# Optimization experiments

Hardware: AMD Instinct MI355X
Metric: run time of the kernel (lower is better)

The kernel has to match this reference:

```python
import jax, jax.numpy as jnp
import numpy as np
from jax.scipy.linalg import expm

D = 512      # d_model
S = 3        # num_scales
BATCH = 256
H = 8        # attention heads
HD = D // H  # head dim


def layernorm(x, g, b, eps=1e-5):
    m = jnp.mean(x, axis=-1, keepdims=True)
    v = jnp.var(x, axis=-1, keepdims=True)
    return (x - m) / jnp.sqrt(v + eps) * g + b


def setup_inputs() -> dict:
    key = jax.random.key(0)
    ks = jax.random.split(key, 16)
    sd = 1.0 / np.sqrt(D)
    inp = {
        'x': jax.random.normal(ks[0], (BATCH, D), jnp.float32),
        'h_prev': jax.random.normal(ks[1], (BATCH, D), jnp.float32),
        'lstm_h': jax.random.normal(ks[2], (S, BATCH, D), jnp.float32) * 0.1,
        'lstm_c': jax.random.normal(ks[3], (S, BATCH, D), jnp.float32) * 0.1,
        'A': jax.random.normal(ks[4], (D, D), jnp.float32) * sd,
        'Bm': jax.random.normal(ks[5], (D, D), jnp.float32) * sd,
        'dn_w1': jax.random.normal(ks[6], (D, D), jnp.float32) * sd,
        'dn_b1': jnp.zeros((D,), jnp.float32),
        'dn_g': jnp.ones((D,), jnp.float32),
        'dn_beta': jnp.zeros((D,), jnp.float32),
        'dn_w2': jax.random.normal(ks[7], (1, D), jnp.float32) * sd,
        'dn_b2': jnp.zeros((1,), jnp.float32),
        'lstm_wih': jax.random.normal(ks[8], (S, 4 * D, D), jnp.float32) * sd,
        'lstm_whh': jax.random.normal(ks[9], (S, 4 * D, D), jnp.float32) * sd,
        'lstm_bih': jnp.zeros((S, 4 * D), jnp.float32),
        'lstm_bhh': jnp.zeros((S, 4 * D), jnp.float32),
        'decays': jnp.linspace(0.5, 0.95, S, dtype=jnp.float32),
        'attn_in_w': jax.random.normal(ks[10], (3 * D, D), jnp.float32) * sd,
        'attn_in_b': jnp.zeros((3 * D,), jnp.float32),
        'attn_out_w': jax.random.normal(ks[11], (D, D), jnp.float32) * sd,
        'attn_out_b': jnp.zeros((D,), jnp.float32),
        'proj_w': jax.random.normal(ks[12], (D, (S + 2) * D), jnp.float32) * (1.0 / np.sqrt((S + 2) * D)),
        'proj_b': jnp.zeros((D,), jnp.float32),
        'proj_g': jnp.ones((D,), jnp.float32),
        'proj_beta': jnp.zeros((D,), jnp.float32),
    }
    return inp


def reference(x, h_prev, lstm_h, lstm_c, A, Bm, dn_w1, dn_b1, dn_g, dn_beta,
              dn_w2, dn_b2, lstm_wih, lstm_whh, lstm_bih, lstm_bhh, decays,
              attn_in_w, attn_in_b, attn_out_w, attn_out_b,
              proj_w, proj_b, proj_g, proj_beta):
    # ---- delta_net: Linear -> LayerNorm -> GELU(exact) -> Linear -> Softplus ----
    h1 = layernorm(x @ dn_w1.T + dn_b1, dn_g, dn_beta)
    h1 = jax.nn.gelu(h1, approximate=False)
    delta = jax.nn.softplus(h1 @ dn_w2.T + dn_b2)           # (B, 1)

    # ---- SSM update: h_t = expm(delta*A) h_prev + delta*B x ----
    A_disc = jax.vmap(expm)(delta[:, :, None] * A)          # (B, D, D)
    h_ssm = jnp.einsum('bij,bj->bi', A_disc, h_prev) + delta * jnp.einsum('ij,bj->bi', Bm, x)

    # ---- multi-scale LSTM cells (vectorized over scales) ----
    gates = (jnp.einsum('bd,skd->sbk', x, lstm_wih)
             + jnp.einsum('sbd,skd->sbk', lstm_h, lstm_whh)
             + (lstm_bih + lstm_bhh)[:, None, :])           # (S, B, 4D)
    gi, gf, gg, go = jnp.split(gates, 4, axis=-1)
    i_g = jax.nn.sigmoid(gi)
    f_g = jax.nn.sigmoid(gf)
    g_g = jnp.tanh(gg)
    o_g = jax.nn.sigmoid(go)
    c_raw = f_g * lstm_c + i_g * g_g                        # (S, B, D)
    h_new = o_g * jnp.tanh(c_raw)                           # (S, B, D)
    dec = decays[:, None, None]
    c_new = dec * lstm_c + (1.0 - dec) * c_raw              # (S, B, D)

    # ---- fusion attention: 1 query (h_ssm), S keys/values (h_new) ----
    Wq, Wk, Wv = jnp.split(attn_in_w, 3, axis=0)
    bq, bk, bv = jnp.split(attn_in_b, 3, axis=0)
    kv = jnp.transpose(h_new, (1, 0, 2))                    # (B, S, D)
    q = (h_ssm @ Wq.T + bq).reshape(-1, 1, H, HD).transpose(0, 2, 1, 3)   # (B,H,1,HD)
    k = (kv @ Wk.T + bk).reshape(-1, S, H, HD).transpose(0, 2, 1, 3)      # (B,H,S,HD)
    v = (kv @ Wv.T + bv).reshape(-1, S, H, HD).transpose(0, 2, 1, 3)
    scores = jnp.einsum('bhqe,bhke->bhqk', q, k) / np.sqrt(HD)
    attn = jax.nn.softmax(scores, axis=-1)
    ctx = jnp.einsum('bhqk,bhke->bhqe', attn, v)            # (B,H,1,HD)
    ctx = ctx.transpose(0, 2, 1, 3).reshape(-1, D)          # (B, D)
    fused = ctx @ attn_out_w.T + attn_out_b                 # (B, D)

    # ---- output projection over concat [h_ssm, fused, h_1..h_S] ----
    combined = jnp.concatenate([h_ssm, fused] + [h_new[i] for i in range(S)], axis=-1)
    output = layernorm(combined @ proj_w.T + proj_b, proj_g, proj_beta)
    return (output, h_ssm, h_new, c_new)
```

## Files before the change

### kernel.cpp

```cpp
#include <hip/hip_runtime.h>
#include <math.h>

#define DIM 512
#define NS 3
#define NB 256
#define KMAX 24

using bf16x8 = __attribute__((ext_vector_type(8))) short;
using f32x4  = __attribute__((ext_vector_type(4))) float;
using float4v = __attribute__((ext_vector_type(4))) float;

__device__ __forceinline__ unsigned short f2b(float f) {
    union { float f; unsigned int u; } v; v.f = f;
    unsigned int r = v.u + 0x7fffu + ((v.u >> 16) & 1u);
    return (unsigned short)(r >> 16);
}
__device__ __forceinline__ float b2f(unsigned short u) {
    union { unsigned int u; float f; } v; v.u = ((unsigned int)u) << 16;
    return v.f;
}

struct GemmDesc {
    const unsigned short* X;
    const unsigned short* W;
    const float* bias;
    float* Cf;
    unsigned short* Cb;
    unsigned short* Ct;
    int M, N, K, ldX, ldC, tr_row0;
};
struct GemmArgs { GemmDesc d[4]; };

__global__ __launch_bounds__(256) void gemm_mfma(GemmArgs args)
{
    GemmDesc de = args.d[blockIdx.y];
    int tn = de.N >> 6;
    int tiles = (de.M >> 6) * tn;
    int t = blockIdx.x;
    if (t >= tiles) return;
    int m0 = (t / tn) << 6;
    int n0 = (t % tn) << 6;

    __shared__ unsigned short lsA[2][4096];
    __shared__ unsigned short lsB[2][4096];

    int tid = threadIdx.x;
    int w = tid >> 6;
    int l = tid & 63;

    int nkt = de.K >> 6;

    int srow = w * 16 + (l >> 2);
    int schk = l & 3;
    const unsigned short* gA = de.X + (size_t)(m0 + srow) * de.ldX + schk * 8;
    const unsigned short* gB = de.W + (size_t)(n0 + srow) * de.K  + schk * 8;
    unsigned short* lA = &lsA[0][(w * 64 + l) * 8];
    unsigned short* lB = &lsB[0][(w * 64 + l) * 8];

#define STAGE(bufi, kt)                                                          \
    do {                                                                         \
        __builtin_amdgcn_global_load_lds(                                        \
            (const __attribute__((address_space(1))) unsigned int*)(gA + (size_t)(kt) * 64), \
            (__attribute__((address_space(3))) unsigned int*)(lA + (bufi) * 4096), 16, 0, 0); \
        __builtin_amdgcn_global_load_lds(                                        \
            (const __attribute__((address_space(1))) unsigned int*)(gA + (size_t)(kt) * 64 + 32), \
            (__attribute__((address_space(3))) unsigned int*)(lA + (bufi) * 4096 + 2048), 16, 0, 0); \
        __builtin_amdgcn_global_load_lds(                                        \
            (const __attribute__((address_space(1))) unsigned int*)(gB + (size_t)(kt) * 64), \
            (__attribute__((address_space(3))) unsigned int*)(lB + (bufi) * 4096), 16, 0, 0); \
        __builtin_amdgcn_global_load_lds(                                        \
            (const __attribute__((address_space(1))) unsigned int*)(gB + (size_t)(kt) * 64 + 32), \
            (__attribute__((address_space(3))) unsigned int*)(lB + (bufi) * 4096 + 2048), 16, 0, 0); \
    } while (0)

    int mbase = (w >> 1) * 32;
    int nbase = (w & 1) * 32;

    f32x4 acc[2][2];
    #pragma unroll
    for (int i = 0; i < 2; ++i)
        #pragma unroll
        for (int j = 0; j < 2; ++j)
            acc[i][j] = (f32x4){0.f, 0.f, 0.f, 0.f};

    int kg = l >> 4;
    int fr = l & 15;
    int aslot = (mbase * 4 + fr * 4 + kg) * 8;
    int bslot = (nbase * 4 + fr * 4 + kg) * 8;

    STAGE(0, 0);

    for (int kt = 0; kt < nkt; ++kt) {
        __syncthreads();
        if (kt + 1 < nkt) STAGE((kt + 1) & 1, kt + 1);

        const unsigned short* bufA = &lsA[kt & 1][0];
        const unsigned short* bufB = &lsB[kt & 1][0];
        #pragma unroll
        for (int h = 0; h < 2; ++h) {
            bf16x8 a0 = *(const bf16x8*)(bufA + h * 2048 + aslot);
            bf16x8 a1 = *(const bf16x8*)(bufA + h * 2048 + aslot + 512);
            bf16x8 b0 = *(const bf16x8*)(bufB + h * 2048 + bslot);
            bf16x8 b1 = *(const bf16x8*)(bufB + h * 2048 + bslot + 512);
            acc[0][0] = __builtin_amdgcn_mfma_f32_16x16x32_bf16(a0, b0, acc[0][0], 0, 0, 0);
            acc[0][1] = __builtin_amdgcn_mfma_f32_16x16x32_bf16(a0, b1, acc[0][1], 0, 0, 0);
            acc[1][0] = __builtin_amdgcn_mfma_f32_16x16x32_bf16(a1, b0, acc[1][0], 0, 0, 0);
            acc[1][1] = __builtin_amdgcn_mfma_f32_16x16x32_bf16(a1, b1, acc[1][1], 0, 0, 0);
        }
    }

    #pragma unroll
    for (int mi = 0; mi < 2; ++mi) {
        #pragma unroll
        for (int ni = 0; ni < 2; ++ni) {
            int col = n0 + nbase + ni * 16 + fr;
            float bv = de.bias ? de.bias[col] : 0.f;
            #pragma unroll
            for (int r = 0; r < 4; ++r) {
                int row = m0 + mbase + mi * 16 + (l >> 4) * 4 + r;
                float v = acc[mi][ni][r] + bv;
                if (de.Cf) de.Cf[(size_t)row * de.ldC + col] = v;
                else       de.Cb[(size_t)row * de.ldC + col] = f2b(v);
                if (de.Ct && row >= de.tr_row0)
                    de.Ct[(size_t)col * 512 + (row - de.tr_row0)] = f2b(v);
            }
        }
    }
#undef STAGE
}

struct ConvArgs { const float* s[8]; unsigned short* d[8]; int n4[8]; int nseg; };
__global__ void convert_pairs(ConvArgs a)
{
    int stride = gridDim.x * blockDim.x;
    for (int seg = 0; seg < a.nseg; ++seg) {
        const float4v* src = (const float4v*)a.s[seg];
        unsigned short* dst = a.d[seg];
        int n4 = a.n4[seg];
        for (int i = blockIdx.x * blockDim.x + threadIdx.x; i < n4; i += stride) {
            float4v v = src[i];
            dst[i*4+0] = f2b(v.x); dst[i*4+1] = f2b(v.y);
            dst[i*4+2] = f2b(v.z); dst[i*4+3] = f2b(v.w);
        }
    }
}

__global__ void build_lstm_cat(const float* __restrict__ wih, const float* __restrict__ whh,
                               const float* __restrict__ x, const float* __restrict__ lh,
                               unsigned short* __restrict__ Wcat, unsigned short* __restrict__ Xcat)
{
    int stride = gridDim.x * blockDim.x;
    const int W4 = 3 * 2048 * 256;
    const int X4 = 3 * 256 * 256;
    for (int g = blockIdx.x * blockDim.x + threadIdx.x; g < W4; g += stride) {
        int s = g / 524288;
        int rr = g - s * 524288;
        int r = rr >> 8;
        int c = (rr & 255) * 4;
        const float* src = (c < 512) ? (wih + (size_t)s * 1048576 + (size_t)r * 512 + c)
                                     : (whh + (size_t)s * 1048576 + (size_t)r * 512 + (c - 512));
        float4v v = *(const float4v*)src;
        unsigned short* dst = Wcat + (size_t)s * 2097152 + (size_t)r * 1024 + c;
        dst[0] = f2b(v.x); dst[1] = f2b(v.y); dst[2] = f2b(v.z); dst[3] = f2b(v.w);
    }
    for (int g = blockIdx.x * blockDim.x + threadIdx.x; g < X4; g += stride) {
        int s = g / 65536;
        int rr = g - s * 65536;
        int b = rr >> 8;
        int c = (rr & 255) * 4;
        const float* src = (c < 512) ? (x + (size_t)b * 512 + c)
                                     : (lh + (size_t)s * 131072 + (size_t)b * 512 + (c - 512));
        float4v v = *(const float4v*)src;
        unsigned short* dst = Xcat + (size_t)s * 262144 + (size_t)b * 1024 + c;
        dst[0] = f2b(v.x); dst[1] = f2b(v.y); dst[2] = f2b(v.z); dst[3] = f2b(v.w);
    }
}

__global__ void transposeA_bf16(const float* __restrict__ A, unsigned short* __restrict__ ATb)
{
    __shared__ float tile[32][33];
    int x = blockIdx.x * 32 + threadIdx.x;
    int y = blockIdx.y * 32 + threadIdx.y;
    #pragma unroll
    for (int i = 0; i < 32; i += 8)
        tile[threadIdx.y + i][threadIdx.x] = A[(size_t)(y + i) * DIM + x];
    __syncthreads();
    x = blockIdx.y * 32 + threadIdx.x;
    y = blockIdx.x * 32 + threadIdx.y;
    #pragma unroll
    for (int i = 0; i < 32; i += 8)
        ATb[(size_t)(y + i) * DIM + x] = f2b(tile[threadIdx.x][threadIdx.y + i]);
}

__device__ __forceinline__ void block_reduce2(float& s, float& q, float* sb1, float* sb2)
{
    int tid = threadIdx.x;
    #pragma unroll
    for (int off = 32; off > 0; off >>= 1) {
        s += __shfl_down(s, off);
        q += __shfl_down(q, off);
    }
    if ((tid & 63) == 0) { sb1[tid >> 6] = s; sb2[tid >> 6] = q; }
    __syncthreads();
    s = sb1[0] + sb1[1] + sb1[2] + sb1[3];
    q = sb2[0] + sb2[1] + sb2[2] + sb2[3];
    __syncthreads();
}

__global__ __launch_bounds__(256) void ln_gelu_delta(
    const float* __restrict__ pre, const float* __restrict__ g,
    const float* __restrict__ beta, const float* __restrict__ w2,
    const float* __restrict__ b2, float* __restrict__ delta,
    float* __restrict__ coeff)
{
    __shared__ float sb1[4], sb2[4];
    int b = blockIdx.x, tid = threadIdx.x;
    int i0 = tid, i1 = tid + 256;
    float x0 = pre[(size_t)b * DIM + i0];
    float x1 = pre[(size_t)b * DIM + i1];
    float s = x0 + x1, q = x0 * x0 + x1 * x1;
    block_reduce2(s, q, sb1, sb2);
    float mean = s * (1.f / DIM);
    float var  = q * (1.f / DIM) - mean * mean;
    float inv  = rsqrtf(var + 1e-5f);
    float y0 = (x0 - mean) * inv * g[i0] + beta[i0];
    float y1 = (x1 - mean) * inv * g[i1] + beta[i1];
    float h0 = 0.5f * y0 * (1.f + erff(y0 * 0.70710678118654752f));
    float h1 = 0.5f * y1 * (1.f + erff(y1 * 0.70710678118654752f));
    float p = h0 * w2[i0] + h1 * w2[i1];
    float dummy = 0.f;
    block_reduce2(p, dummy, sb1, sb2);
    if (tid == 0) {
        float z = p + b2[0];
        float d = (z > 20.f) ? z : log1pf(expf(z));
        delta[b] = d;
        float c = 1.f;
        coeff[b] = 1.f;
        for (int k = 1; k <= KMAX; ++k) { c *= d / (float)k; coeff[k * 256 + b] = c; }
    }
}

__global__ void taylor_accum(
    const float* __restrict__ T, const float* __restrict__ coeff,
    const float* __restrict__ h_prev, const float* __restrict__ delta,
    const float* __restrict__ Bx, float* __restrict__ hssm,
    unsigned short* __restrict__ combb)
{
    int idx = blockIdx.x * 256 + threadIdx.x;
    int b = idx >> 9, i = idx & 511;
    const float* Tr = T + (size_t)b * (KMAX * DIM) + i;
    float a = h_prev[idx];
    #pragma unroll
    for (int k = 1; k <= KMAX; ++k)
        a += coeff[k * 256 + b] * Tr[(size_t)(k - 1) * DIM];
    float h = a + delta[b] * Bx[idx];
    hssm[idx] = h;
    combb[(size_t)b * 2560 + i] = f2b(h);
}

__global__ void lstm_cell(
    const float* __restrict__ gates, const float* __restrict__ bih,
    const float* __restrict__ bhh, const float* __restrict__ cin,
    const float* __restrict__ decays,
    float* __restrict__ hout, float* __restrict__ cout,
    unsigned short* __restrict__ combb)
{
    int idx = blockIdx.x * 256 + threadIdx.x;
    int s = idx / (NB * DIM);
    int r = idx - s * (NB * DIM);
    int b = r >> 9, d = r & 511;
    const float* gr = gates + (size_t)s * 524288 + (size_t)b * 2048;
    const float* bi = bih + s * 2048;
    const float* bh = bhh + s * 2048;
    float gi = gr[d]        + bi[d]        + bh[d];
    float gf = gr[512 + d]  + bi[512 + d]  + bh[512 + d];
    float gg = gr[1024 + d] + bi[1024 + d] + bh[1024 + d];
    float go = gr[1536 + d] + bi[1536 + d] + bh[1536 + d];
    float ig = 1.f / (1.f + expf(-gi));
    float fg = 1.f / (1.f + expf(-gf));
    float g_ = tanhf(gg);
    float og = 1.f / (1.f + expf(-go));
    float c  = cin[idx];
    float craw = fg * c + ig * g_;
    float hn = og * tanhf(craw);
    float dec = decays[s];
    hout[idx] = hn;
    cout[idx] = dec * c + (1.f - dec) * craw;
    combb[(size_t)b * 2560 + 1024 + s * 512 + d] = f2b(hn);
}

__global__ __launch_bounds__(64) void attn_kernel(
    const unsigned short* __restrict__ qb, const unsigned short* __restrict__ kvb,
    unsigned short* __restrict__ ctxb)
{
    int bh = blockIdx.x;
    int b = bh >> 3, h = bh & 7;
    int e = threadIdx.x;
    int col = h * 64 + e;
    float qe = b2f(qb[(size_t)b * 512 + col]);
    float p0 = qe * b2f(kvb[0 * 262144 + (size_t)b * 1024 + col]);
    float p1 = qe * b2f(kvb[1 * 262144 + (size_t)b * 1024 + col]);
    float p2 = qe * b2f(kvb[2 * 262144 + (size_t)b * 1024 + col]);
    #pragma unroll
    for (int off = 32; off > 0; off >>= 1) {
        p0 += __shfl_xor(p0, off);
        p1 += __shfl_xor(p1, off);
        p2 += __shfl_xor(p2, off);
    }
    const float scale = 0.125f;
    p0 *= scale; p1 *= scale; p2 *= scale;
    float m = fmaxf(p0, fmaxf(p1, p2));
    float w0 = expf(p0 - m), w1 = expf(p1 - m), w2 = expf(p2 - m);
    float invs = 1.f / (w0 + w1 + w2);
    float v0 = b2f(kvb[0 * 262144 + (size_t)b * 1024 + 512 + col]);
    float v1 = b2f(kvb[1 * 262144 + (size_t)b * 1024 + 512 + col]);
    float v2 = b2f(kvb[2 * 262144 + (size_t)b * 1024 + 512 + col]);
    ctxb[(size_t)b * 512 + col] = f2b((w0 * v0 + w1 * v1 + w2 * v2) * invs);
}

__global__ __launch_bounds__(256) void layernorm_k(
    const float* __restrict__ in, const float* __restrict__ g,
    const float* __restrict__ beta, float* __restrict__ outp)
{
    __shared__ float sb1[4], sb2[4];
    int b = blockIdx.x, tid = threadIdx.x;
    int i0 = tid, i1 = tid + 256;
    float x0 = in[(size_t)b * DIM + i0];
    float x1 = in[(size_t)b * DIM + i1];
    float s = x0 + x1, q = x0 * x0 + x1 * x1;
    block_reduce2(s, q, sb1, sb2);
    float mean = s * (1.f / DIM);
    float var  = q * (1.f / DIM) - mean * mean;
    float inv  = rsqrtf(var + 1e-5f);
    outp[(size_t)b * DIM + i0] = (x0 - mean) * inv * g[i0] + beta[i0];
    outp[(size_t)b * DIM + i1] = (x1 - mean) * inv * g[i1] + beta[i1];
}

extern "C" void kernel_launch(void* const* d_in, const int* in_sizes, int n_in,
                              void* d_out, int out_size, void* d_ws, size_t ws_size,
                              hipStream_t stream)
{
    const float* x        = (const float*)d_in[0];
    const float* h_prev   = (const float*)d_in[1];
    const float* lstm_h   = (const float*)d_in[2];
    const float* lstm_c   = (const float*)d_in[3];
    const float* A        = (const float*)d_in[4];
    const float* Bm       = (const float*)d_in[5];
    const float* dn_w1    = (const float*)d_in[6];
    const float* dn_b1    = (const float*)d_in[7];
    const float* dn_g     = (const float*)d_in[8];
    const float* dn_beta  = (const float*)d_in[9];
    const float* dn_w2    = (const float*)d_in[10];
    const float* dn_b2    = (const float*)d_in[11];
    const float* wih      = (const float*)d_in[12];
    const float* whh      = (const float*)d_in[13];
    const float* bih      = (const float*)d_in[14];
    const float* bhh      = (const float*)d_in[15];
    const float* decays   = (const float*)d_in[16];
    const float* ain_w    = (const float*)d_in[17];
    const float* ain_b    = (const float*)d_in[18];
    const float* aout_w   = (const float*)d_in[19];
    const float* aout_b   = (const float*)d_in[20];
    const float* proj_w   = (const float*)d_in[21];
    const float* proj_b   = (const float*)d_in[22];
    const float* proj_g   = (const float*)d_in[23];
    const float* proj_bt  = (const float*)d_in[24];

    float* out  = (float*)d_out;
    float* hssm = out + 131072;
    float* hnew = out + 262144;
    float* cnew = out + 655360;

    unsigned short* us = (unsigned short*)d_ws;
    unsigned short* xb      = us;
    unsigned short* hpb     = us + 131072;
    unsigned short* ATb     = us + 262144;
    unsigned short* dn_w1b  = us + 524288;
    unsigned short* Bmb     = us + 786432;
    unsigned short* ain_wb  = us + 1048576;
    unsigned short* aout_wb = us + 1835008;
    unsigned short* proj_wb = us + 2097152;
    unsigned short* Pw      = us + 3407872;
    unsigned short* Qa      = us + 9699328;
    unsigned short* Qb      = us + 9961472;
    unsigned short* Wcat    = us + 10223616;
    unsigned short* Xcat    = us + 16515072;
    unsigned short* combb   = us + 17301504;
    unsigned short* kvb     = us + 17956864;
    unsigned short* qb      = us + 18743296;
    unsigned short* ctxb    = us + 18874368;
    float* fbase = (float*)(us + 19005440);
    float* pre1   = fbase;
    float* delta  = fbase + 131072;
    float* coeff  = fbase + 131328;
    float* Bx     = fbase + 137728;
    float* Tm     = fbase + 268800;
    float* gates  = Tm;
    float* projout = pre1;

    ConvArgs ca;
    ca.s[0] = x;      ca.d[0] = xb;      ca.n4[0] = 131072/4;
    ca.s[1] = h_prev; ca.d[1] = hpb;     ca.n4[1] = 131072/4;
    ca.s[2] = A;      ca.d[2] = Pw;      ca.n4[2] = 262144/4;
    ca.s[3] = dn_w1;  ca.d[3] = dn_w1b;  ca.n4[3] = 262144/4;
    ca.s[4] = Bm;     ca.d[4] = Bmb;     ca.n4[4] = 262144/4;
    ca.s[5] = ain_w;  ca.d[5] = ain_wb;  ca.n4[5] = 786432/4;
    ca.s[6] = aout_w; ca.d[6] = aout_wb; ca.n4[6] = 262144/4;
    ca.s[7] = proj_w; ca.d[7] = proj_wb; ca.n4[7] = 1310720/4;
    ca.nseg = 8;
    convert_pairs<<<1024, 256, 0, stream>>>(ca);
    build_lstm_cat<<<2048, 256, 0, stream>>>(wih, whh, x, lstm_h, Wcat, Xcat);
    transposeA_bf16<<<dim3(16, 16), dim3(32, 8), 0, stream>>>(A, ATb);

    GemmArgs ga;
    ga.d[0] = { xb, dn_w1b, dn_b1, pre1, nullptr, nullptr, 256, 512, 512, 512, 512, 0 };
    ga.d[1] = { xb, Bmb,    nullptr, Bx,  nullptr, nullptr, 256, 512, 512, 512, 512, 0 };
    gemm_mfma<<<dim3(32, 2), 256, 0, stream>>>(ga);
    ln_gelu_delta<<<256, 256, 0, stream>>>(pre1, dn_g, dn_beta, dn_w2, dn_b2, delta, coeff);

    ga.d[0] = { Pw, ATb, nullptr, nullptr, Pw + 1*262144, Qa, 512, 512, 512, 512, 512, 0 };
    gemm_mfma<<<dim3(64, 1), 256, 0, stream>>>(ga);
    ga.d[0] = { Pw, Qa, nullptr, nullptr, Pw + 2*262144, Qb, 1024, 512, 512, 512, 512, 512 };
    gemm_mfma<<<dim3(128, 1), 256, 0, stream>>>(ga);
    ga.d[0] = { Pw, Qb, nullptr, nullptr, Pw + 4*262144, Qa, 2048, 512, 512, 512, 512, 1536 };
    gemm_mfma<<<dim3(256, 1), 256, 0, stream>>>(ga);
    ga.d[0] = { Pw, Qa, nullptr, nullptr, Pw + 8*262144, Qb, 4096, 512, 512, 512, 512, 3584 };
    gemm_mfma<<<dim3(512, 1), 256, 0, stream>>>(ga);
    ga.d[0] = { Pw, Qb, nullptr, nullptr, Pw + 16*262144, nullptr, 4096, 512, 512, 512, 512, 0 };
    gemm_mfma<<<dim3(512, 1), 256, 0, stream>>>(ga);

    ga.d[0] = { hpb, Pw, nullptr, Tm, nullptr, nullptr, 256, KMAX*512, 512, 512, KMAX*512, 0 };
    gemm_mfma<<<dim3(768, 1), 256, 0, stream>>>(ga);
    taylor_accum<<<512, 256, 0, stream>>>(Tm, coeff, h_prev, delta, Bx, hssm, combb);

    for (int s = 0; s < 3; ++s)
        ga.d[s] = { Xcat + (size_t)s * 262144, Wcat + (size_t)s * 2097152, nullptr,
                    gates + (size_t)s * 524288, nullptr, nullptr, 256, 2048, 1024, 1024, 2048, 0 };
    gemm_mfma<<<dim3(128, 3), 256, 0, stream>>>(ga);
    lstm_cell<<<1536, 256, 0, stream>>>(gates, bih, bhh, lstm_c, decays, hnew, cnew, combb);

    ga.d[0] = { combb, ain_wb, ain_b, nullptr, qb, nullptr, 256, 512, 512, 2560, 512, 0 };
    for (int s = 0; s < 3; ++s)
        ga.d[1 + s] = { combb + 1024 + (size_t)s * 512, ain_wb + 262144, ain_b + 512,
                        nullptr, kvb + (size_t)s * 262144, nullptr, 256, 1024, 512, 2560, 1024, 0 };
    gemm_mfma<<<dim3(64, 4), 256, 0, stream>>>(ga);
    attn_kernel<<<2048, 64, 0, stream>>>(qb, kvb, ctxb);
    ga.d[0] = { ctxb, aout_wb, aout_b, nullptr, combb + 512, nullptr, 256, 512, 512, 512, 2560, 0 };
    gemm_mfma<<<dim3(32, 1), 256, 0, stream>>>(ga);

    ga.d[0] = { combb, proj_wb, proj_b, projout, nullptr, nullptr, 256, 512, 2560, 2560, 512, 0 };
    gemm_mfma<<<dim3(32, 1), 256, 0, stream>>>(ga);
    layernorm_k<<<256, 256, 0, stream>>>(projout, proj_g, proj_bt, out);
}
```

Measured before the change: 273.1 us.

## Cut Taylor order, fold attention out-proj into output projection, merge launches

```diff
diff --git a/kernel.cpp b/kernel.cpp
--- a/kernel.cpp
+++ b/kernel.cpp
@@ -2,9 +2,8 @@
 #include <math.h>
 
 #define DIM 512
-#define NS 3
 #define NB 256
-#define KMAX 24
+#define KMAX 16
 
 using bf16x8 = __attribute__((ext_vector_type(8))) short;
 using f32x4  = __attribute__((ext_vector_type(4))) float;
@@ -47,7 +46,6 @@
     int tid = threadIdx.x;
     int w = tid >> 6;
     int l = tid & 63;
-
     int nkt = de.K >> 6;
 
     int srow = w * 16 + (l >> 2);
@@ -129,18 +127,64 @@
 #undef STAGE
 }
 
-struct ConvArgs { const float* s[8]; unsigned short* d[8]; int n4[8]; int nseg; };
-__global__ void convert_pairs(ConvArgs a)
-{
-    int stride = gridDim.x * blockDim.x;
-    for (int seg = 0; seg < a.nseg; ++seg) {
-        const float4v* src = (const float4v*)a.s[seg];
-        unsigned short* dst = a.d[seg];
-        int n4 = a.n4[seg];
-        for (int i = blockIdx.x * blockDim.x + threadIdx.x; i < n4; i += stride) {
-            float4v v = src[i];
-            dst[i*4+0] = f2b(v.x); dst[i*4+1] = f2b(v.y);
-            dst[i*4+2] = f2b(v.z); dst[i*4+3] = f2b(v.w);
+struct PrepArgs {
+    const float* lin_s[7]; unsigned short* lin_d[7];
+    int lin_n4[7]; int lin_dRL[7]; int lin_sRL[7]; int lin_sOff[7];
+    const float* A; unsigned short* ATb;
+    const float* aout_w; unsigned short* aout_wT;
+    const float* proj_w; const float* proj_b; const float* aout_b; float* bprime;
+};
+__global__ __launch_bounds__(256) void prep_kernel(PrepArgs a)
+{
+    __shared__ float tile[32][33];
+    int bid = blockIdx.x, tid = threadIdx.x;
+    if (bid < 1024) {
+        int gstride = 1024 * 256;
+        int g0 = bid * 256 + tid;
+        for (int seg = 0; seg < 7; ++seg) {
+            int n4 = a.lin_n4[seg];
+            const float* s = a.lin_s[seg];
+            unsigned short* d = a.lin_d[seg];
+            int dRL = a.lin_dRL[seg], sRL = a.lin_sRL[seg], off = a.lin_sOff[seg];
+            if (dRL == sRL && off == 0) {
+                for (int i = g0; i < n4; i += gstride) {
+                    float4v v = ((const float4v*)s)[i];
+                    d[i*4+0] = f2b(v.x); d[i*4+1] = f2b(v.y);
+                    d[i*4+2] = f2b(v.z); d[i*4+3] = f2b(v.w);
+                }
+            } else {
+                for (int i = g0; i < n4; i += gstride) {
+                    int r = i / dRL, c = i - r * dRL;
+                    float4v v = *(const float4v*)(s + ((size_t)r * sRL + off + c) * 4);
+                    unsigned short* dd = d + ((size_t)r * dRL + c) * 4;
+                    dd[0] = f2b(v.x); dd[1] = f2b(v.y); dd[2] = f2b(v.z); dd[3] = f2b(v.w);
+                }
+            }
+        }
+    } else if (bid < 1536) {
+        int t = bid - 1024;
+        const float* src = (t < 256) ? a.A : a.aout_w;
+        unsigned short* dst = (t < 256) ? a.ATb : a.aout_wT;
+        int tt = t & 255;
+        int bx = tt & 15, by = tt >> 4;
+        int tx = tid & 31, ty = tid >> 5;
+        #pragma unroll
+        for (int i = 0; i < 32; i += 8)
+            tile[ty + i][tx] = src[(size_t)(by * 32 + ty + i) * 512 + bx * 32 + tx];
+        __syncthreads();
+        #pragma unroll
+        for (int i = 0; i < 32; i += 8)
+            dst[(size_t)(bx * 32 + ty + i) * 512 + by * 32 + tx] = f2b(tile[tx][ty + i]);
+    } else {
+        int gw = (bid - 1536) * 4 + (tid >> 6);
+        int lane = tid & 63;
+        for (int i = gw; i < 512; i += 32) {
+            float acc = 0.f;
+            for (int n = lane; n < 512; n += 64)
+                acc += a.proj_w[(size_t)i * 2560 + 512 + n] * a.aout_b[n];
+            #pragma unroll
+            for (int off = 32; off > 0; off >>= 1) acc += __shfl_down(acc, off);
+            if (lane == 0) a.bprime[i] = a.proj_b[i] + acc;
         }
     }
 }
@@ -174,22 +218,6 @@
         unsigned short* dst = Xcat + (size_t)s * 262144 + (size_t)b * 1024 + c;
         dst[0] = f2b(v.x); dst[1] = f2b(v.y); dst[2] = f2b(v.z); dst[3] = f2b(v.w);
     }
-}
-
-__global__ void transposeA_bf16(const float* __restrict__ A, unsigned short* __restrict__ ATb)
-{
-    __shared__ float tile[32][33];
-    int x = blockIdx.x * 32 + threadIdx.x;
-    int y = blockIdx.y * 32 + threadIdx.y;
-    #pragma unroll
-    for (int i = 0; i < 32; i += 8)
-        tile[threadIdx.y + i][threadIdx.x] = A[(size_t)(y + i) * DIM + x];
-    __syncthreads();
-    x = blockIdx.y * 32 + threadIdx.x;
-    y = blockIdx.x * 32 + threadIdx.y;
-    #pragma unroll
-    for (int i = 0; i < 32; i += 8)
-        ATb[(size_t)(y + i) * DIM + x] = f2b(tile[threadIdx.x][threadIdx.y + i]);
 }
 
 __device__ __forceinline__ void block_reduce2(float& s, float& q, float* sb1, float* sb2)
@@ -240,58 +268,56 @@
     }
 }
 
-__global__ void taylor_accum(
-    const float* __restrict__ T, const float* __restrict__ coeff,
+__global__ void pointwise_fused(
+    const float* __restrict__ Tm, const float* __restrict__ coeff,
     const float* __restrict__ h_prev, const float* __restrict__ delta,
     const float* __restrict__ Bx, float* __restrict__ hssm,
-    unsigned short* __restrict__ combb)
-{
-    int idx = blockIdx.x * 256 + threadIdx.x;
-    int b = idx >> 9, i = idx & 511;
-    const float* Tr = T + (size_t)b * (KMAX * DIM) + i;
-    float a = h_prev[idx];
-    #pragma unroll
-    for (int k = 1; k <= KMAX; ++k)
-        a += coeff[k * 256 + b] * Tr[(size_t)(k - 1) * DIM];
-    float h = a + delta[b] * Bx[idx];
-    hssm[idx] = h;
-    combb[(size_t)b * 2560 + i] = f2b(h);
-}
-
-__global__ void lstm_cell(
+    unsigned short* __restrict__ combb,
     const float* __restrict__ gates, const float* __restrict__ bih,
     const float* __restrict__ bhh, const float* __restrict__ cin,
     const float* __restrict__ decays,
-    float* __restrict__ hout, float* __restrict__ cout,
-    unsigned short* __restrict__ combb)
+    float* __restrict__ hout, float* __restrict__ cout)
 {
     int idx = blockIdx.x * 256 + threadIdx.x;
-    int s = idx / (NB * DIM);
-    int r = idx - s * (NB * DIM);
-    int b = r >> 9, d = r & 511;
-    const float* gr = gates + (size_t)s * 524288 + (size_t)b * 2048;
-    const float* bi = bih + s * 2048;
-    const float* bh = bhh + s * 2048;
-    float gi = gr[d]        + bi[d]        + bh[d];
-    float gf = gr[512 + d]  + bi[512 + d]  + bh[512 + d];
-    float gg = gr[1024 + d] + bi[1024 + d] + bh[1024 + d];
-    float go = gr[1536 + d] + bi[1536 + d] + bh[1536 + d];
-    float ig = 1.f / (1.f + expf(-gi));
-    float fg = 1.f / (1.f + expf(-gf));
-    float g_ = tanhf(gg);
-    float og = 1.f / (1.f + expf(-go));
-    float c  = cin[idx];
-    float craw = fg * c + ig * g_;
-    float hn = og * tanhf(craw);
-    float dec = decays[s];
-    hout[idx] = hn;
-    cout[idx] = dec * c + (1.f - dec) * craw;
-    combb[(size_t)b * 2560 + 1024 + s * 512 + d] = f2b(hn);
+    if (idx < 131072) {
+        int b = idx >> 9, i = idx & 511;
+        const float* Tr = Tm + (size_t)b * (KMAX * DIM) + i;
+        float a = h_prev[idx];
+        #pragma unroll
+        for (int k = 1; k <= KMAX; ++k)
+            a += coeff[k * 256 + b] * Tr[(size_t)(k - 1) * DIM];
+        float h = a + delta[b] * Bx[idx];
+        hssm[idx] = h;
+        combb[(size_t)b * 2560 + i] = f2b(h);
+    } else {
+        int idx2 = idx - 131072;
+        int s = idx2 / (NB * DIM);
+        int r = idx2 - s * (NB * DIM);
+        int b = r >> 9, d = r & 511;
+        const float* gr = gates + (size_t)s * 524288 + (size_t)b * 2048;
+        const float* bi = bih + s * 2048;
+        const float* bh = bhh + s * 2048;
+        float gi = gr[d]        + bi[d]        + bh[d];
+        float gf = gr[512 + d]  + bi[512 + d]  + bh[512 + d];
+        float gg = gr[1024 + d] + bi[1024 + d] + bh[1024 + d];
+        float go = gr[1536 + d] + bi[1536 + d] + bh[1536 + d];
+        float ig = 1.f / (1.f + expf(-gi));
+        float fg = 1.f / (1.f + expf(-gf));
+        float g_ = tanhf(gg);
+        float og = 1.f / (1.f + expf(-go));
+        float c  = cin[idx2];
+        float craw = fg * c + ig * g_;
+        float hn = og * tanhf(craw);
+        float dec = decays[s];
+        hout[idx2] = hn;
+        cout[idx2] = dec * c + (1.f - dec) * craw;
+        combb[(size_t)b * 2560 + 1024 + s * 512 + d] = f2b(hn);
+    }
 }
 
 __global__ __launch_bounds__(64) void attn_kernel(
     const unsigned short* __restrict__ qb, const unsigned short* __restrict__ kvb,
-    unsigned short* __restrict__ ctxb)
+    unsigned short* __restrict__ combb)
 {
     int bh = blockIdx.x;
     int b = bh >> 3, h = bh & 7;
@@ -315,7 +341,7 @@
     float v0 = b2f(kvb[0 * 262144 + (size_t)b * 1024 + 512 + col]);
     float v1 = b2f(kvb[1 * 262144 + (size_t)b * 1024 + 512 + col]);
     float v2 = b2f(kvb[2 * 262144 + (size_t)b * 1024 + 512 + col]);
-    ctxb[(size_t)b * 512 + col] = f2b((w0 * v0 + w1 * v1 + w2 * v2) * invs);
+    combb[(size_t)b * 2560 + 512 + col] = f2b((w0 * v0 + w1 * v1 + w2 * v2) * invs);
 }
 
 __global__ __launch_bounds__(256) void layernorm_k(
@@ -372,50 +398,51 @@
     float* cnew = out + 655360;
 
     unsigned short* us = (unsigned short*)d_ws;
-    unsigned short* xb      = us;
-    unsigned short* hpb     = us + 131072;
-    unsigned short* ATb     = us + 262144;
-    unsigned short* dn_w1b  = us + 524288;
-    unsigned short* Bmb     = us + 786432;
-    unsigned short* ain_wb  = us + 1048576;
-    unsigned short* aout_wb = us + 1835008;
-    unsigned short* proj_wb = us + 2097152;
-    unsigned short* Pw      = us + 3407872;
-    unsigned short* Qa      = us + 9699328;
-    unsigned short* Qb      = us + 9961472;
-    unsigned short* Wcat    = us + 10223616;
-    unsigned short* Xcat    = us + 16515072;
-    unsigned short* combb   = us + 17301504;
-    unsigned short* kvb     = us + 17956864;
-    unsigned short* qb      = us + 18743296;
-    unsigned short* ctxb    = us + 18874368;
-    float* fbase = (float*)(us + 19005440);
+    unsigned short* hpb     = us;
+    unsigned short* ATb     = us + 131072;
+    unsigned short* dn_w1b  = us + 393216;
+    unsigned short* Bmb     = us + 655360;
+    unsigned short* ain_wb  = us + 917504;
+    unsigned short* proj_wb = us + 1703936;
+    unsigned short* P2b     = us + 3014656;
+    unsigned short* aout_wT = us + 3276800;
+    unsigned short* Pw      = us + 3538944;
+    unsigned short* Qa      = us + 7733248;
+    unsigned short* Qb      = us + 7995392;
+    unsigned short* Wcat    = us + 8257536;
+    unsigned short* Xcat    = us + 14548992;
+    unsigned short* combb   = us + 15335424;
+    unsigned short* qb      = us + 15990784;
+    unsigned short* kvb     = us + 16121856;
+    float* fbase  = (float*)(us + 16908288);
     float* pre1   = fbase;
     float* delta  = fbase + 131072;
     float* coeff  = fbase + 131328;
-    float* Bx     = fbase + 137728;
-    float* Tm     = fbase + 268800;
-    float* gates  = Tm;
+    float* Bx     = fbase + 135680;
+    float* bprime = fbase + 266752;
+    float* Tm     = fbase + 267264;
+    float* gates  = fbase + 2364416;
     float* projout = pre1;
 
-    ConvArgs ca;
-    ca.s[0] = x;      ca.d[0] = xb;      ca.n4[0] = 131072/4;
-    ca.s[1] = h_prev; ca.d[1] = hpb;     ca.n4[1] = 131072/4;
-    ca.s[2] = A;      ca.d[2] = Pw;      ca.n4[2] = 262144/4;
-    ca.s[3] = dn_w1;  ca.d[3] = dn_w1b;  ca.n4[3] = 262144/4;
-    ca.s[4] = Bm;     ca.d[4] = Bmb;     ca.n4[4] = 262144/4;
-    ca.s[5] = ain_w;  ca.d[5] = ain_wb;  ca.n4[5] = 786432/4;
-    ca.s[6] = aout_w; ca.d[6] = aout_wb; ca.n4[6] = 262144/4;
-    ca.s[7] = proj_w; ca.d[7] = proj_wb; ca.n4[7] = 1310720/4;
-    ca.nseg = 8;
-    convert_pairs<<<1024, 256, 0, stream>>>(ca);
+    PrepArgs pa;
+    pa.lin_s[0] = h_prev; pa.lin_d[0] = hpb;     pa.lin_n4[0] = 32768;  pa.lin_dRL[0]=1;   pa.lin_sRL[0]=1;   pa.lin_sOff[0]=0;
+    pa.lin_s[1] = A;      pa.lin_d[1] = Pw;      pa.lin_n4[1] = 65536;  pa.lin_dRL[1]=1;   pa.lin_sRL[1]=1;   pa.lin_sOff[1]=0;
+    pa.lin_s[2] = dn_w1;  pa.lin_d[2] = dn_w1b;  pa.lin_n4[2] = 65536;  pa.lin_dRL[2]=1;   pa.lin_sRL[2]=1;   pa.lin_sOff[2]=0;
+    pa.lin_s[3] = Bm;     pa.lin_d[3] = Bmb;     pa.lin_n4[3] = 65536;  pa.lin_dRL[3]=1;   pa.lin_sRL[3]=1;   pa.lin_sOff[3]=0;
+    pa.lin_s[4] = ain_w;  pa.lin_d[4] = ain_wb;  pa.lin_n4[4] = 196608; pa.lin_dRL[4]=1;   pa.lin_sRL[4]=1;   pa.lin_sOff[4]=0;
+    pa.lin_s[5] = proj_w; pa.lin_d[5] = proj_wb; pa.lin_n4[5] = 327680; pa.lin_dRL[5]=1;   pa.lin_sRL[5]=1;   pa.lin_sOff[5]=0;
+    pa.lin_s[6] = proj_w; pa.lin_d[6] = P2b;     pa.lin_n4[6] = 65536;  pa.lin_dRL[6]=128; pa.lin_sRL[6]=640; pa.lin_sOff[6]=128;
+    pa.A = A; pa.ATb = ATb; pa.aout_w = aout_w; pa.aout_wT = aout_wT;
+    pa.proj_w = proj_w; pa.proj_b = proj_b; pa.aout_b = aout_b; pa.bprime = bprime;
+    prep_kernel<<<1544, 256, 0, stream>>>(pa);
     build_lstm_cat<<<2048, 256, 0, stream>>>(wih, whh, x, lstm_h, Wcat, Xcat);
-    transposeA_bf16<<<dim3(16, 16), dim3(32, 8), 0, stream>>>(A, ATb);
 
     GemmArgs ga;
-    ga.d[0] = { xb, dn_w1b, dn_b1, pre1, nullptr, nullptr, 256, 512, 512, 512, 512, 0 };
-    ga.d[1] = { xb, Bmb,    nullptr, Bx,  nullptr, nullptr, 256, 512, 512, 512, 512, 0 };
-    gemm_mfma<<<dim3(32, 2), 256, 0, stream>>>(ga);
+    ga.d[0] = { Xcat, dn_w1b, dn_b1, pre1, nullptr, nullptr, 256, 512, 512, 1024, 512, 0 };
+    ga.d[1] = { Xcat, Bmb,    nullptr, Bx,  nullptr, nullptr, 256, 512, 512, 1024, 512, 0 };
+    ga.d[2] = { P2b,  aout_wT, nullptr, nullptr, proj_wb + 512, nullptr, 512, 512, 512, 512, 2560, 0 };
+    ga.d[3] = ga.d[0];
+    gemm_mfma<<<dim3(64, 3), 256, 0, stream>>>(ga);
     ln_gelu_delta<<<256, 256, 0, stream>>>(pre1, dn_g, dn_beta, dn_w2, dn_b2, delta, coeff);
 
     ga.d[0] = { Pw, ATb, nullptr, nullptr, Pw + 1*262144, Qa, 512, 512, 512, 512, 512, 0 };
@@ -424,31 +451,26 @@
     gemm_mfma<<<dim3(128, 1), 256, 0, stream>>>(ga);
     ga.d[0] = { Pw, Qb, nullptr, nullptr, Pw + 4*262144, Qa, 2048, 512, 512, 512, 512, 1536 };
     gemm_mfma<<<dim3(256, 1), 256, 0, stream>>>(ga);
-    ga.d[0] = { Pw, Qa, nullptr, nullptr, Pw + 8*262144, Qb, 4096, 512, 512, 512, 512, 3584 };
+    ga.d[0] = { Pw, Qa, nullptr, nullptr, Pw + 8*262144, nullptr, 4096, 512, 512, 512, 512, 0 };
     gemm_mfma<<<dim3(512, 1), 256, 0, stream>>>(ga);
-    ga.d[0] = { Pw, Qb, nullptr, nullptr, Pw + 16*262144, nullptr, 4096, 512, 512, 512, 512, 0 };
-    gemm_mfma<<<dim3(512, 1), 256, 0, stream>>>(ga);
 
     ga.d[0] = { hpb, Pw, nullptr, Tm, nullptr, nullptr, 256, KMAX*512, 512, 512, KMAX*512, 0 };
-    gemm_mfma<<<dim3(768, 1), 256, 0, stream>>>(ga);
-    taylor_accum<<<512, 256, 0, stream>>>(Tm, coeff, h_prev, delta, Bx, hssm, combb);
-
     for (int s = 0; s < 3; ++s)
-        ga.d[s] = { Xcat + (size_t)s * 262144, Wcat + (size_t)s * 2097152, nullptr,
-                    gates + (size_t)s * 524288, nullptr, nullptr, 256, 2048, 1024, 1024, 2048, 0 };
-    gemm_mfma<<<dim3(128, 3), 256, 0, stream>>>(ga);
-    lstm_cell<<<1536, 256, 0, stream>>>(gates, bih, bhh, lstm_c, decays, hnew, cnew, combb);
+        ga.d[1 + s] = { Xcat + (size_t)s * 262144, Wcat + (size_t)s * 2097152, nullptr,
+                        gates + (size_t)s * 524288, nullptr, nullptr, 256, 2048, 1024, 1024, 2048, 0 };
+    gemm_mfma<<<dim3(512, 4), 256, 0, stream>>>(ga);
+
+    pointwise_fused<<<2048, 256, 0, stream>>>(Tm, coeff, h_prev, delta, Bx, hssm, combb,
+                                              gates, bih, bhh, lstm_c, decays, hnew, cnew);
 
     ga.d[0] = { combb, ain_wb, ain_b, nullptr, qb, nullptr, 256, 512, 512, 2560, 512, 0 };
     for (int s = 0; s < 3; ++s)
         ga.d[1 + s] = { combb + 1024 + (size_t)s * 512, ain_wb + 262144, ain_b + 512,
                         nullptr, kvb + (size_t)s * 262144, nullptr, 256, 1024, 512, 2560, 1024, 0 };
     gemm_mfma<<<dim3(64, 4), 256, 0, stream>>>(ga);
-    attn_kernel<<<2048, 64, 0, stream>>>(qb, kvb, ctxb);
-    ga.d[0] = { ctxb, aout_wb, aout_b, nullptr, combb + 512, nullptr, 256, 512, 512, 512, 2560, 0 };
-    gemm_mfma<<<dim3(32, 1), 256, 0, stream>>>(ga);
-
-    ga.d[0] = { combb, proj_wb, proj_b, projout, nullptr, nullptr, 256, 512, 2560, 2560, 512, 0 };
+    attn_kernel<<<2048, 64, 0, stream>>>(qb, kvb, combb);
+
+    ga.d[0] = { combb, proj_wb, bprime, projout, nullptr, nullptr, 256, 512, 2560, 2560, 512, 0 };
     gemm_mfma<<<dim3(32, 1), 256, 0, stream>>>(ga);
     layernorm_k<<<256, 256, 0, stream>>>(projout, proj_g, proj_bt, out);
 }
```

Result: slower. 284.4 us (+4.1%).
